# Kernel tuning notes

Measured on AMD Instinct MI355X. Metric: run time of the kernel, lower is better.

## Reference

```python
import jax, jax.numpy as jnp
import numpy as np

D = 256          # d_model
NPRE = 16; NMLP = 16; NPOST = 16
K = 4            # top_k
P = NPRE * NMLP * NPOST   # 4096 pathways
HMAX = 5 * D     # max mlp expert hidden width (padded storage)
B, S = 8, 256


def _gelu(z):
    return jax.nn.gelu(z, approximate=False)  # torch nn.GELU default = exact erf


def _ln(z, g, b, eps=1e-5):
    mu = z.mean(-1, keepdims=True)
    v = ((z - mu) ** 2).mean(-1, keepdims=True)
    return (z - mu) * jax.lax.rsqrt(v + eps) * g + b


def setup_inputs() -> dict:
    key = jax.random.key(0)
    ks = jax.random.split(key, 8)

    def nrm(k, shape, scale):
        return jax.random.normal(k, shape, dtype=jnp.float32) * scale

    return {
        "x": nrm(ks[0], (B, S, D), 1.0),
        # router MLP (dropout inactive in eval)
        "rw1": nrm(ks[1], (D, 256), D ** -0.5), "rb1": jnp.zeros((256,), jnp.float32),
        "rw2": nrm(ks[2], (256, 128), 256 ** -0.5), "rb2": jnp.zeros((128,), jnp.float32),
        "rw3": nrm(ks[3], (128, P), 128 ** -0.5), "rb3": jnp.zeros((P,), jnp.float32),
        "temp": jnp.ones((1,), jnp.float32),
        # pre experts: Linear + LayerNorm + act
        "pw": nrm(ks[4], (NPRE, D, D), D ** -0.5), "pb": jnp.zeros((NPRE, D), jnp.float32),
        "pg": jnp.ones((NPRE, D), jnp.float32), "pbb": jnp.zeros((NPRE, D), jnp.float32),
        # mlp experts: variable hidden D*(2+i//4), padded to HMAX (unused cols sliced off)
        "mw1": nrm(ks[5], (NMLP, D, HMAX), D ** -0.5), "mb1": jnp.zeros((NMLP, HMAX), jnp.float32),
        "mw2": nrm(ks[6], (NMLP, HMAX, D), HMAX ** -0.5), "mb2": jnp.zeros((NMLP, D), jnp.float32),
        # post experts: Linear + (LayerNorm if even)
        "qw": nrm(ks[7], (NPOST, D, D), D ** -0.5), "qb": jnp.zeros((NPOST, D), jnp.float32),
        "qg": jnp.ones((NPOST, D), jnp.float32), "qbb": jnp.zeros((NPOST, D), jnp.float32),
    }


def reference(x, rw1, rb1, rw2, rb2, rw3, rb3, temp, pw, pb, pg, pbb,
              mw1, mb1, mw2, mb2, qw, qb, qg, qbb):
    Bv, Sv, Dv = x.shape
    N = Bv * Sv
    xt = x.reshape(N, Dv)

    # ---- router ----
    h = _gelu(xt @ rw1 + rb1)
    h = _gelu(h @ rw2 + rb2)
    scores = h @ rw3 + rb3                                  # [N, P]

    # ---- GLBL load-balance loss (softmax without temperature; torch.var unbiased) ----
    freq = jax.nn.softmax(scores, axis=-1).mean(0)          # [P]
    glbl_loss = P * jnp.var(freq, ddof=1)

    # ---- top-k pathway selection ----
    probs = jax.nn.softmax(scores / temp[0], axis=-1)
    top_vals, top_idx = jax.lax.top_k(probs, K)             # [N, K]
    pw_full = jnp.zeros((N, P), x.dtype).at[jnp.arange(N)[:, None], top_idx].set(top_vals)
    pathway_weights = pw_full / (pw_full.sum(-1, keepdims=True) + 1e-8)

    # ---- decompose pathway index -> (pre, mlp, post) ----
    pre_idx = top_idx // (NMLP * NPOST)
    rem = top_idx % (NMLP * NPOST)
    mlp_idx = rem // NPOST
    post_idx = rem % NPOST

    # ---- pre experts: compute all, gather per (token, slot) ----
    acts = [_gelu, jax.nn.relu, jnp.tanh]
    pre_all = jnp.stack(
        [acts[i % 3](_ln(xt @ pw[i] + pb[i], pg[i], pbb[i])) for i in range(NPRE)],
        axis=1)                                              # [N, NPRE, D]
    x_pre = jnp.take_along_axis(pre_all, pre_idx[:, :, None], axis=1)  # [N, K, D]

    # ---- mlp experts (variable hidden width), masked combine ----
    x_mlp = jnp.zeros_like(x_pre)
    for j in range(NMLP):
        hid = Dv * (2 + j // 4)
        a = _gelu if j % 2 == 0 else jax.nn.relu
        mid = a(jnp.einsum('nkd,dh->nkh', x_pre, mw1[j, :, :hid]) + mb1[j, :hid])
        out = jnp.einsum('nkh,hd->nkd', mid, mw2[j, :hid, :]) + mb2[j]
        x_mlp = x_mlp + jnp.where((mlp_idx == j)[:, :, None], out, 0.0)

    # ---- post experts, masked combine ----
    x_post = jnp.zeros_like(x_mlp)
    for q in range(NPOST):
        out = jnp.einsum('nkd,de->nke', x_mlp, qw[q]) + qb[q]
        if q % 2 == 0:
            out = _ln(out, qg[q], qbb[q])
        x_post = x_post + jnp.where((post_idx == q)[:, :, None], out, 0.0)

    # original weights each pathway by its (unnormalized) top value
    output = (x_post * top_vals[:, :, None]).sum(1).reshape(Bv, Sv, Dv)
    return output, glbl_loss, pathway_weights.reshape(Bv, Sv, P)
```

## Files before the change

### kernel.cpp

```cpp
#include <hip/hip_runtime.h>
#include <math.h>

#define DMODEL 256
#define PWAYS  4096
#define TOPK   4
#define HMAX   1280
#define NTOK   2048
#define NPAIR  (NTOK*TOPK)
#define FSLOTS 16
#define TILE   16
#define YBLK   64
#define MROWS  64
#define YMLP   8
#define CTOT   56

typedef __attribute__((ext_vector_type(8))) short bf16x8;
typedef __attribute__((ext_vector_type(8))) unsigned short u16x8;
typedef __attribute__((ext_vector_type(4))) float f32x4;

#define MFMA_BF16 __builtin_amdgcn_mfma_f32_16x16x32_bf16

__device__ __forceinline__ float gelu_exact(float z) {
    return 0.5f * z * (1.0f + erff(z * 0.70710678118654752440f));
}

__device__ __forceinline__ unsigned short f32_to_bf16_rne(float f) {
    unsigned u = __float_as_uint(f);
    unsigned r = u + 0x7FFFu + ((u >> 16) & 1u);
    return (unsigned short)(r >> 16);
}

__device__ __forceinline__ float bf16_to_f32(unsigned short h) {
    return __uint_as_float((unsigned)h << 16);
}

__device__ __forceinline__ int chunk_base(int e) {
    int g = e >> 2, r = e & 3;
    return 4 * (2 * g + (g * (g - 1)) / 2) + r * (2 + g);
}


__global__ void k_zero(float* __restrict__ pwout, float* __restrict__ freq_part) {
    const int i = blockIdx.x * 256 + threadIdx.x;
    const int stride = gridDim.x * 256;
    for (int j = i; j < NTOK * PWAYS; j += stride) pwout[j] = 0.0f;
    for (int j = i; j < FSLOTS * PWAYS; j += stride) freq_part[j] = 0.0f;
}

__global__ void k_zero2(float* __restrict__ out, float* __restrict__ x_mlp,
                        int* __restrict__ cnts) {
    const int i = blockIdx.x * 256 + threadIdx.x;
    const int stride = gridDim.x * 256;
    for (int j = i; j < NTOK * DMODEL; j += stride) out[j] = 0.0f;
    for (int j = i; j < NPAIR * DMODEL; j += stride) x_mlp[j] = 0.0f;
    if (i < 192) cnts[i] = 0;
}

__global__ void __launch_bounds__(256) k_router_h(
    const float* __restrict__ x,
    const float* __restrict__ rw1, const float* __restrict__ rb1,
    const float* __restrict__ rw2, const float* __restrict__ rb2,
    unsigned short* __restrict__ h2h, unsigned short* __restrict__ h2l) {
    __shared__ float xs[4][DMODEL];
    __shared__ float h1s[4][DMODEL];
    __shared__ float h2s[4][128];
    const int tid = threadIdx.x;
    const int n0 = blockIdx.x * 4;

    for (int idx = tid; idx < 4 * DMODEL; idx += 256)
        xs[idx >> 8][idx & 255] = x[(size_t)n0 * DMODEL + idx];
    __syncthreads();

    {
        float bias = rb1[tid];
        float a0 = bias, a1 = bias, a2 = bias, a3 = bias;
        for (int c = 0; c < DMODEL; c++) {
            float wv = rw1[c * DMODEL + tid];
            a0 += xs[0][c] * wv; a1 += xs[1][c] * wv;
            a2 += xs[2][c] * wv; a3 += xs[3][c] * wv;
        }
        h1s[0][tid] = gelu_exact(a0); h1s[1][tid] = gelu_exact(a1);
        h1s[2][tid] = gelu_exact(a2); h1s[3][tid] = gelu_exact(a3);
    }
    __syncthreads();

    {
        const int col = tid & 127;
        const int pr = tid >> 7;
        float bias = rb2[col];
        float b0 = bias, b1 = bias;
        for (int c = 0; c < DMODEL; c++) {
            float wv = rw2[c * 128 + col];
            b0 += h1s[2 * pr + 0][c] * wv;
            b1 += h1s[2 * pr + 1][c] * wv;
        }
        h2s[2 * pr + 0][col] = gelu_exact(b0);
        h2s[2 * pr + 1][col] = gelu_exact(b1);
    }
    __syncthreads();

    for (int idx = tid; idx < 512; idx += 256) {
        const int t = idx >> 7, col = idx & 127;
        const float v = h2s[t][col];
        const unsigned short h = f32_to_bf16_rne(v);
        const size_t o = (size_t)(n0 + t) * 128 + col;
        h2h[o] = h;
        h2l[o] = f32_to_bf16_rne(v - bf16_to_f32(h));
    }
}

__global__ void __launch_bounds__(256) k_pack3(
    const float* __restrict__ rw3, unsigned short* __restrict__ P3) {
    const int nb = blockIdx.x;
    const int tid = threadIdx.x;
    const int kb = tid >> 6, lane = tid & 63;
    const int l15 = lane & 15, lhi = lane >> 4;
    const int k0 = kb * 32 + lhi * 8;
    const int n = nb * 16 + l15;
    u16x8 hv, lv;
#pragma unroll
    for (int j = 0; j < 8; ++j) {
        const float f = rw3[(size_t)(k0 + j) * PWAYS + n];
        const unsigned short h = f32_to_bf16_rne(f);
        hv[j] = h;
        lv[j] = f32_to_bf16_rne(f - bf16_to_f32(h));
    }
    const size_t o0 = ((size_t)(0 * 256 + nb) * 4 + kb) * 512 + (size_t)lane * 8;
    const size_t o1 = ((size_t)(1 * 256 + nb) * 4 + kb) * 512 + (size_t)lane * 8;
    *(u16x8*)&P3[o0] = hv;
    *(u16x8*)&P3[o1] = lv;
}

__global__ void __launch_bounds__(256, 2) k_scores(
    const unsigned short* __restrict__ h2h, const unsigned short* __restrict__ h2l,
    const unsigned short* __restrict__ P3, const float* __restrict__ rb3,
    float* __restrict__ scores) {
    const int n0 = blockIdx.x * 32;
    const int by = blockIdx.y;
    const int tid = threadIdx.x;
    const int wid = tid >> 6, lane = tid & 63;
    const int l15 = lane & 15, lhi = lane >> 4;

    __shared__ unsigned short ah[32][136];
    __shared__ unsigned short al[32][136];

    for (int t = tid; t < 512; t += 256) {
        const int row = t >> 4, seg = (t & 15) * 8;
        const size_t g = (size_t)(n0 + row) * 128 + seg;
        *(u16x8*)&ah[row][seg] = *(const u16x8*)&h2h[g];
        *(u16x8*)&al[row][seg] = *(const u16x8*)&h2l[g];
    }
    __syncthreads();

    f32x4 acc[2][4];
    const f32x4 zf = {0.f, 0.f, 0.f, 0.f};
#pragma unroll
    for (int ms = 0; ms < 2; ++ms)
#pragma unroll
        for (int ns = 0; ns < 4; ++ns) acc[ms][ns] = zf;

#pragma unroll 1
    for (int kb = 0; kb < 4; ++kb) {
        const int ko = kb * 32 + lhi * 8;
        const bf16x8 a_h0 = *(const bf16x8*)&ah[l15][ko];
        const bf16x8 a_h1 = *(const bf16x8*)&ah[16 + l15][ko];
        const bf16x8 a_l0 = *(const bf16x8*)&al[l15][ko];
        const bf16x8 a_l1 = *(const bf16x8*)&al[16 + l15][ko];
#pragma unroll
        for (int ns = 0; ns < 4; ++ns) {
            const int nb = by * 16 + wid * 4 + ns;
            const size_t bo = ((size_t)nb * 4 + kb) * 512 + (size_t)lane * 8;
            const bf16x8 bh = *(const bf16x8*)&P3[bo];
            const bf16x8 bl = *(const bf16x8*)&P3[bo + 524288];
            acc[0][ns] = MFMA_BF16(a_h0, bh, acc[0][ns], 0, 0, 0);
            acc[1][ns] = MFMA_BF16(a_h1, bh, acc[1][ns], 0, 0, 0);
            acc[0][ns] = MFMA_BF16(a_l0, bh, acc[0][ns], 0, 0, 0);
            acc[1][ns] = MFMA_BF16(a_l1, bh, acc[1][ns], 0, 0, 0);
            acc[0][ns] = MFMA_BF16(a_h0, bl, acc[0][ns], 0, 0, 0);
            acc[1][ns] = MFMA_BF16(a_h1, bl, acc[1][ns], 0, 0, 0);
        }
    }

#pragma unroll
    for (int ms = 0; ms < 2; ++ms)
#pragma unroll
        for (int ns = 0; ns < 4; ++ns) {
            const int col = by * 256 + wid * 64 + ns * 16 + l15;
            const float bias = rb3[col];
#pragma unroll
            for (int r = 0; r < 4; ++r) {
                const int row = n0 + ms * 16 + lhi * 4 + r;
                scores[(size_t)row * PWAYS + col] = acc[ms][ns][r] + bias;
            }
        }
}

__global__ void __launch_bounds__(256) k_topk(
    const float* __restrict__ scores, const float* __restrict__ temp,
    int* __restrict__ top_idx, float* __restrict__ top_vals,
    float* __restrict__ pw_out, float* __restrict__ tok_m, float* __restrict__ tok_i) {
    const int n = blockIdx.x;
    const int tid = threadIdx.x;
    const int wid = tid >> 6, lane = tid & 63;
    const float* row = scores + (size_t)n * PWAYS;

    float sv[16];
#pragma unroll
    for (int i = 0; i < 16; ++i) sv[i] = row[tid + i * 256];

    __shared__ float wred[4];
    __shared__ float wr1[4], wrT[4];
    __shared__ float wbv[4];
    __shared__ int wbi[4];
    __shared__ int sel[TOPK];
    __shared__ float selv[TOPK];

    float lmax = -3.402823466e38f;
#pragma unroll
    for (int i = 0; i < 16; ++i) lmax = fmaxf(lmax, sv[i]);
    for (int o = 32; o > 0; o >>= 1) lmax = fmaxf(lmax, __shfl_down(lmax, o));
    if (lane == 0) wred[wid] = lmax;
    __syncthreads();
    const float m = fmaxf(fmaxf(wred[0], wred[1]), fmaxf(wred[2], wred[3]));

    const float invT = 1.0f / temp[0];
    float e1 = 0.f, eT = 0.f;
#pragma unroll
    for (int i = 0; i < 16; ++i) {
        const float d = sv[i] - m;
        e1 += expf(d);
        eT += expf(d * invT);
    }
    for (int o = 32; o > 0; o >>= 1) { e1 += __shfl_down(e1, o); eT += __shfl_down(eT, o); }
    if (lane == 0) { wr1[wid] = e1; wrT[wid] = eT; }
    __syncthreads();
    const float sum1 = wr1[0] + wr1[1] + wr1[2] + wr1[3];
    const float sumT = wrT[0] + wrT[1] + wrT[2] + wrT[3];

    for (int r = 0; r < TOPK; ++r) {
        float bv = -3.402823466e38f;
        int bi = PWAYS;
#pragma unroll
        for (int i = 0; i < 16; ++i) {
            const int p = tid + i * 256;
            bool skip = false;
            for (int u = 0; u < r; ++u) if (sel[u] == p) skip = true;
            if (!skip && sv[i] > bv) { bv = sv[i]; bi = p; }
        }
        for (int o = 32; o > 0; o >>= 1) {
            const float ov = __shfl_down(bv, o);
            const int oi = __shfl_down(bi, o);
            if (ov > bv || (ov == bv && oi < bi)) { bv = ov; bi = oi; }
        }
        if (lane == 0) { wbv[wid] = bv; wbi[wid] = bi; }
        __syncthreads();
        if (tid == 0) {
            float b = wbv[0]; int bidx = wbi[0];
            for (int w = 1; w < 4; ++w)
                if (wbv[w] > b || (wbv[w] == b && wbi[w] < bidx)) { b = wbv[w]; bidx = wbi[w]; }
            sel[r] = bidx; selv[r] = b;
        }
        __syncthreads();
    }

    if (tid == 0) {
        float tv[TOPK];
        float wsum = 1e-8f;
#pragma unroll
        for (int k2 = 0; k2 < TOPK; ++k2) {
            tv[k2] = expf((selv[k2] - m) * invT) / sumT;
            wsum += tv[k2];
        }
        const float invw = 1.0f / wsum;
#pragma unroll
        for (int k2 = 0; k2 < TOPK; ++k2) {
            top_idx[n * TOPK + k2] = sel[k2];
            top_vals[n * TOPK + k2] = tv[k2];
            pw_out[(size_t)n * PWAYS + sel[k2]] = tv[k2] * invw;
        }
        tok_m[n] = m;
        tok_i[n] = 1.0f / sum1;
    }
}

__global__ void __launch_bounds__(256) k_freq(
    const float* __restrict__ scores, const float* __restrict__ tok_m,
    const float* __restrict__ tok_i, float* __restrict__ freq_part) {
    const int bx = blockIdx.x;
    const int by = blockIdx.y;
    const int tid = threadIdx.x;
    const int wid = tid >> 6, lane = tid & 63;
    const int col = bx * 64 + lane;

    float acc = 0.f;
    const int r0 = by * 128;
    for (int r = r0 + wid; r < r0 + 128; r += 4) {
        const float mm = tok_m[r], iv = tok_i[r];
        acc += expf(scores[(size_t)r * PWAYS + col] - mm) * iv;
    }
    __shared__ float fs[4][64];
    fs[wid][lane] = acc;
    __syncthreads();
    if (wid == 0)
        freq_part[(size_t)by * PWAYS + col] = fs[0][lane] + fs[1][lane] + fs[2][lane] + fs[3][lane];
}

__global__ void k_freq_loss(const float* __restrict__ freq_part, float* __restrict__ out_loss) {
    __shared__ float fl[PWAYS];
    __shared__ float red[256];
    const int tid = threadIdx.x;
    for (int p = tid; p < PWAYS; p += 256) {
        float s = 0.f;
        for (int sl = 0; sl < FSLOTS; sl++) s += freq_part[(size_t)sl * PWAYS + p];
        fl[p] = s * (1.0f / NTOK);
    }
    __syncthreads();
    float s = 0.f;
    for (int p = tid; p < PWAYS; p += 256) s += fl[p];
    red[tid] = s; __syncthreads();
    for (int st = 128; st > 0; st >>= 1) { if (tid < st) red[tid] += red[tid + st]; __syncthreads(); }
    const float mu = red[0] * (1.0f / PWAYS);
    __syncthreads();
    float ss = 0.f;
    for (int p = tid; p < PWAYS; p += 256) {
        float d = fl[p] - mu;
        ss += d * d;
    }
    red[tid] = ss; __syncthreads();
    for (int st = 128; st > 0; st >>= 1) { if (tid < st) red[tid] += red[tid + st]; __syncthreads(); }
    if (tid == 0)
        out_loss[0] = (float)PWAYS * red[0] / (float)(PWAYS - 1);
}


__global__ void k_count(const int* __restrict__ top_idx, int* __restrict__ counts) {
    const int p = blockIdx.x * 256 + threadIdx.x;
    if (p >= NPAIR) return;
    const int idx = top_idx[p];
    atomicAdd(&counts[0 * 16 + (idx >> 8)], 1);
    atomicAdd(&counts[1 * 16 + ((idx >> 4) & 15)], 1);
    atomicAdd(&counts[2 * 16 + (idx & 15)], 1);
}

__global__ void k_prefix(const int* __restrict__ counts, int* __restrict__ offsets,
                         int* __restrict__ cursors) {
    if (threadIdx.x != 0 || blockIdx.x != 0) return;
    for (int s = 0; s < 3; s++) {
        int run = 0;
        for (int e = 0; e < 16; e++) {
            offsets[s * 16 + e] = run;
            cursors[s * 16 + e] = run;
            run += counts[s * 16 + e];
        }
    }
}

__global__ void k_scatter(const int* __restrict__ top_idx, int* __restrict__ cursors,
                          int* __restrict__ lists) {
    const int p = blockIdx.x * 256 + threadIdx.x;
    if (p >= NPAIR) return;
    const int idx = top_idx[p];
    int pos;
    pos = atomicAdd(&cursors[0 * 16 + (idx >> 8)], 1);        lists[0 * NPAIR + pos] = p;
    pos = atomicAdd(&cursors[1 * 16 + ((idx >> 4) & 15)], 1); lists[1 * NPAIR + pos] = p;
    pos = atomicAdd(&cursors[2 * 16 + (idx & 15)], 1);        lists[2 * NPAIR + pos] = p;
}

__device__ __forceinline__ void wave_stats(const float* row, int lane,
                                           float& s1, float& s2) {
    float v0 = row[lane], v1 = row[lane + 64], v2 = row[lane + 128], v3 = row[lane + 192];
    s1 = v0 + v1 + v2 + v3;
    s2 = v0 * v0 + v1 * v1 + v2 * v2 + v3 * v3;
    for (int o = 32; o > 0; o >>= 1) {
        s1 += __shfl_down(s1, o);
        s2 += __shfl_down(s2, o);
    }
}

__global__ void __launch_bounds__(256) k_packw(
    const float* __restrict__ mw1, const float* __restrict__ mw2,
    unsigned short* __restrict__ W1P, unsigned short* __restrict__ W2P) {
    const int cl = blockIdx.x;
    const int which = blockIdx.y;
    const int kb = blockIdx.z;
    int e = 0;
    while (e < 15 && chunk_base(e + 1) <= cl) ++e;
    const int ch = cl - chunk_base(e);
    const int hbase = ch * 256;
    const int tid = threadIdx.x;
    const int wid = tid >> 6, lane = tid & 63;
    const int l15 = lane & 15, lhi = lane >> 4;

    unsigned short* dst = which ? W2P : W1P;

    for (int nb = wid; nb < 16; nb += 4) {
        const int n = nb * 16 + l15;
        const int k0 = kb * 32 + lhi * 8;
        u16x8 hv, lv;
#pragma unroll
        for (int j = 0; j < 8; ++j) {
            float f;
            if (which == 0)
                f = mw1[((size_t)e * DMODEL + (k0 + j)) * HMAX + hbase + n];
            else
                f = mw2[((size_t)e * HMAX + hbase + k0 + j) * DMODEL + n];
            const unsigned short h = f32_to_bf16_rne(f);
            hv[j] = h;
            lv[j] = f32_to_bf16_rne(f - bf16_to_f32(h));
        }
        const size_t o0 = ((((size_t)cl * 2 + 0) * 16 + nb) * 8 + kb) * 512 + (size_t)lane * 8;
        const size_t o1 = ((((size_t)cl * 2 + 1) * 16 + nb) * 8 + kb) * 512 + (size_t)lane * 8;
        *(u16x8*)&dst[o0] = hv;
        *(u16x8*)&dst[o1] = lv;
    }
}

__global__ void __launch_bounds__(256, 8) k_pre(
    const float* __restrict__ x, const float* __restrict__ pw, const float* __restrict__ pb,
    const float* __restrict__ pg, const float* __restrict__ pbb,
    const int* __restrict__ counts, const int* __restrict__ offsets,
    const int* __restrict__ lists,
    unsigned short* __restrict__ x_h, unsigned short* __restrict__ x_l) {
    const int e = blockIdx.x;
    const int cnt = counts[e];
    const int off = offsets[e];
    const int tid = threadIdx.x;
    const float bias = pb[e * DMODEL + tid];
    const float g = pg[e * DMODEL + tid], bb = pbb[e * DMODEL + tid];
    const int am = e % 3;
    const float* W = pw + (size_t)e * DMODEL * DMODEL + tid;

    __shared__ int prs[TILE];
    __shared__ float buf[TILE][DMODEL];
    __shared__ float mus[TILE], ivs[TILE];

    for (int base = blockIdx.y * TILE; base < cnt; base += YBLK * TILE) {
        const int Tact = min(TILE, cnt - base);
        if (tid < TILE) prs[tid] = lists[off + base + ((tid < Tact) ? tid : (Tact - 1))];
        __syncthreads();
#pragma unroll
        for (int j = 0; j < TILE; j++)
            buf[j][tid] = x[(size_t)(prs[j] >> 2) * DMODEL + tid];
        __syncthreads();

        float acc[TILE];
#pragma unroll
        for (int j = 0; j < TILE; j++) acc[j] = bias;
        for (int c = 0; c < DMODEL; c += 4) {
            const float w0 = W[(c + 0) * DMODEL], w1 = W[(c + 1) * DMODEL];
            const float w2 = W[(c + 2) * DMODEL], w3 = W[(c + 3) * DMODEL];
#pragma unroll
            for (int j = 0; j < TILE; j++) {
                float4 xv = *(const float4*)&buf[j][c];
                acc[j] += xv.x * w0 + xv.y * w1 + xv.z * w2 + xv.w * w3;
            }
        }
        __syncthreads();
#pragma unroll
        for (int j = 0; j < TILE; j++) buf[j][tid] = acc[j];
        __syncthreads();

        const int w = tid >> 6, lane = tid & 63;
        for (int i = 0; i < 4; i++) {
            const int j = w * 4 + i;
            float s1, s2;
            wave_stats(buf[j], lane, s1, s2);
            if (lane == 0) {
                float mu = s1 * (1.0f / DMODEL);
                mus[j] = mu;
                ivs[j] = rsqrtf(s2 * (1.0f / DMODEL) - mu * mu + 1e-5f);
            }
        }
        __syncthreads();

        for (int j = 0; j < Tact; j++) {
            float y = (acc[j] - mus[j]) * ivs[j] * g + bb;
            y = (am == 0) ? gelu_exact(y) : (am == 1 ? fmaxf(y, 0.f) : tanhf(y));
            const unsigned short h = f32_to_bf16_rne(y);
            const size_t o = (size_t)prs[j] * DMODEL + tid;
            x_h[o] = h;
            x_l[o] = f32_to_bf16_rne(y - bf16_to_f32(h));
        }
        __syncthreads();
    }
}

__global__ void __launch_bounds__(256, 2) k_mlp_mfma(
    const unsigned short* __restrict__ x_h, const unsigned short* __restrict__ x_l,
    const unsigned short* __restrict__ W1P, const unsigned short* __restrict__ W2P,
    const float* __restrict__ mb1, const float* __restrict__ mb2,
    const int* __restrict__ counts, const int* __restrict__ offsets,
    const int* __restrict__ lists, float* __restrict__ x_mlp) {
    const int p = blockIdx.x & 7;
    const int j = blockIdx.x >> 3;
    const int ea = p;
    const int eb = (p < 4) ? (p + 12) : (p + 4);
    const int na = (2 + (ea >> 2)) * YMLP;
    int e, ch, y;
    if (j < na) { e = ea; ch = j >> 3; y = j & 7; }
    else        { e = eb; ch = (j - na) >> 3; y = (j - na) & 7; }

    const int cnt = counts[16 + e];
    if (cnt == 0) return;
    const int off = offsets[16 + e];
    const int cl = chunk_base(e) + ch;
    const bool is_gelu = ((e & 1) == 0);
    const int tid = threadIdx.x;
    const int wid = tid >> 6, lane = tid & 63;
    const int l15 = lane & 15, lhi = lane >> 4;

    __shared__ int prs[MROWS];
    __shared__ unsigned short ah[MROWS][264];
    __shared__ unsigned short al[MROWS][264];

    float hb_s[4], ob_s[4];
#pragma unroll
    for (int ns = 0; ns < 4; ++ns) {
        const int col = wid * 64 + ns * 16 + l15;
        hb_s[ns] = mb1[e * HMAX + ch * DMODEL + col];
        ob_s[ns] = (ch == 0) ? mb2[e * DMODEL + col] : 0.0f;
    }

    const size_t wbase = (size_t)cl * 2 * 65536;

    for (int base = y * MROWS; base < cnt; base += YMLP * MROWS) {
        const int Tact = min(MROWS, cnt - base);
        if (tid < MROWS) prs[tid] = lists[NPAIR + off + base + min(tid, Tact - 1)];
        __syncthreads();
        for (int t = tid; t < 2048; t += 256) {
            const int row = t >> 5, seg = (t & 31) * 8;
            const size_t gsrc = (size_t)prs[row] * DMODEL + seg;
            *(uint4*)&ah[row][seg] = *(const uint4*)&x_h[gsrc];
            *(uint4*)&al[row][seg] = *(const uint4*)&x_l[gsrc];
        }
        __syncthreads();

        {
            f32x4 acc[4][4];
            const f32x4 zf = {0.f, 0.f, 0.f, 0.f};
#pragma unroll
            for (int ms = 0; ms < 4; ++ms)
#pragma unroll
                for (int ns = 0; ns < 4; ++ns) acc[ms][ns] = zf;

#pragma unroll 1
            for (int kb = 0; kb < 8; ++kb) {
                const int ko = kb * 32 + lhi * 8;
#pragma unroll
                for (int ns = 0; ns < 4; ++ns) {
                    const size_t bo = wbase + (size_t)(((wid * 4 + ns) * 8 + kb) * 512 + lane * 8);
                    const bf16x8 bh = *(const bf16x8*)&W1P[bo];
                    const bf16x8 bl = *(const bf16x8*)&W1P[bo + 65536];
#pragma unroll
                    for (int ms = 0; ms < 4; ++ms) {
                        const bf16x8 a_h = *(const bf16x8*)&ah[ms * 16 + l15][ko];
                        const bf16x8 a_l = *(const bf16x8*)&al[ms * 16 + l15][ko];
                        acc[ms][ns] = MFMA_BF16(a_h, bh, acc[ms][ns], 0, 0, 0);
                        acc[ms][ns] = MFMA_BF16(a_l, bh, acc[ms][ns], 0, 0, 0);
                        acc[ms][ns] = MFMA_BF16(a_h, bl, acc[ms][ns], 0, 0, 0);
                    }
                }
            }
            __syncthreads();

#pragma unroll
            for (int ms = 0; ms < 4; ++ms)
#pragma unroll
                for (int ns = 0; ns < 4; ++ns) {
                    const int col = wid * 64 + ns * 16 + l15;
#pragma unroll
                    for (int r = 0; r < 4; ++r) {
                        const int row = ms * 16 + lhi * 4 + r;
                        float v = acc[ms][ns][r] + hb_s[ns];
                        v = is_gelu ? gelu_exact(v) : fmaxf(v, 0.0f);
                        const unsigned short h = f32_to_bf16_rne(v);
                        ah[row][col] = h;
                        al[row][col] = f32_to_bf16_rne(v - bf16_to_f32(h));
                    }
                }
            __syncthreads();
        }

        {
            f32x4 acc2[4][4];
            const f32x4 zf = {0.f, 0.f, 0.f, 0.f};
#pragma unroll
            for (int ms = 0; ms < 4; ++ms)
#pragma unroll
                for (int ns = 0; ns < 4; ++ns) acc2[ms][ns] = zf;

#pragma unroll 1
            for (int kb = 0; kb < 8; ++kb) {
                const int ko = kb * 32 + lhi * 8;
#pragma unroll
                for (int ns = 0; ns < 4; ++ns) {
                    const size_t bo = wbase + (size_t)(((wid * 4 + ns) * 8 + kb) * 512 + lane * 8);
                    const bf16x8 bh = *(const bf16x8*)&W2P[bo];
                    const bf16x8 bl = *(const bf16x8*)&W2P[bo + 65536];
#pragma unroll
                    for (int ms = 0; ms < 4; ++ms) {
                        const bf16x8 a_h = *(const bf16x8*)&ah[ms * 16 + l15][ko];
                        const bf16x8 a_l = *(const bf16x8*)&al[ms * 16 + l15][ko];
                        acc2[ms][ns] = MFMA_BF16(a_h, bh, acc2[ms][ns], 0, 0, 0);
                        acc2[ms][ns] = MFMA_BF16(a_l, bh, acc2[ms][ns], 0, 0, 0);
                        acc2[ms][ns] = MFMA_BF16(a_h, bl, acc2[ms][ns], 0, 0, 0);
                    }
                }
            }

#pragma unroll
            for (int ms = 0; ms < 4; ++ms)
#pragma unroll
                for (int ns = 0; ns < 4; ++ns) {
                    const int col = wid * 64 + ns * 16 + l15;
#pragma unroll
                    for (int r = 0; r < 4; ++r) {
                        const int row = ms * 16 + lhi * 4 + r;
                        if (row < Tact)
                            atomicAdd(&x_mlp[(size_t)prs[row] * DMODEL + col],
                                      acc2[ms][ns][r] + ob_s[ns]);
                    }
                }
        }
        __syncthreads();
    }
}

__global__ void __launch_bounds__(256, 8) k_post(
    const float* __restrict__ x_mlp,
    const float* __restrict__ qw, const float* __restrict__ qb,
    const float* __restrict__ qg, const float* __restrict__ qbb,
    const float* __restrict__ top_val,
    const int* __restrict__ counts, const int* __restrict__ offsets,
    const int* __restrict__ lists, float* __restrict__ out) {
    const int e = blockIdx.x;
    const int cnt = counts[32 + e];
    const int off = offsets[32 + e];
    const int tid = threadIdx.x;
    const float bias = qb[e * DMODEL + tid];
    const bool has_ln = ((e & 1) == 0);
    const float g = has_ln ? qg[e * DMODEL + tid] : 0.f;
    const float bb = has_ln ? qbb[e * DMODEL + tid] : 0.f;
    const float* W = qw + (size_t)e * DMODEL * DMODEL + tid;

    __shared__ int prs[TILE];
    __shared__ float tvs[TILE];
    __shared__ float buf[TILE][DMODEL];
    __shared__ float mus[TILE], ivs[TILE];

    for (int base = blockIdx.y * TILE; base < cnt; base += YBLK * TILE) {
        const int Tact = min(TILE, cnt - base);
        if (tid < TILE) {
            int p = lists[2 * NPAIR + off + base + ((tid < Tact) ? tid : (Tact - 1))];
            prs[tid] = p;
            tvs[tid] = top_val[p];
        }
        __syncthreads();
#pragma unroll
        for (int j = 0; j < TILE; j++)
            buf[j][tid] = x_mlp[(size_t)prs[j] * DMODEL + tid];
        __syncthreads();

        float acc[TILE];
#pragma unroll
        for (int j = 0; j < TILE; j++) acc[j] = bias;
        for (int c = 0; c < DMODEL; c += 4) {
            const float w0 = W[(c + 0) * DMODEL], w1 = W[(c + 1) * DMODEL];
            const float w2 = W[(c + 2) * DMODEL], w3 = W[(c + 3) * DMODEL];
#pragma unroll
            for (int j = 0; j < TILE; j++) {
                float4 xv = *(const float4*)&buf[j][c];
                acc[j] += xv.x * w0 + xv.y * w1 + xv.z * w2 + xv.w * w3;
            }
        }

        if (has_ln) {
            __syncthreads();
#pragma unroll
            for (int j = 0; j < TILE; j++) buf[j][tid] = acc[j];
            __syncthreads();
            const int w = tid >> 6, lane = tid & 63;
            for (int i = 0; i < 4; i++) {
                const int j = w * 4 + i;
                float s1, s2;
                wave_stats(buf[j], lane, s1, s2);
                if (lane == 0) {
                    float mu = s1 * (1.0f / DMODEL);
                    mus[j] = mu;
                    ivs[j] = rsqrtf(s2 * (1.0f / DMODEL) - mu * mu + 1e-5f);
                }
            }
            __syncthreads();
            for (int j = 0; j < Tact; j++) {
                float t = (acc[j] - mus[j]) * ivs[j] * g + bb;
                atomicAdd(&out[(size_t)(prs[j] >> 2) * DMODEL + tid], tvs[j] * t);
            }
        } else {
            for (int j = 0; j < Tact; j++)
                atomicAdd(&out[(size_t)(prs[j] >> 2) * DMODEL + tid], tvs[j] * acc[j]);
        }
        __syncthreads();
    }
}

extern "C" void kernel_launch(void* const* d_in, const int* in_sizes, int n_in,
                              void* d_out, int out_size, void* d_ws, size_t ws_size,
                              hipStream_t stream) {
    (void)in_sizes; (void)n_in; (void)out_size; (void)ws_size;

    const float* x    = (const float*)d_in[0];
    const float* rw1  = (const float*)d_in[1];
    const float* rb1  = (const float*)d_in[2];
    const float* rw2  = (const float*)d_in[3];
    const float* rb2  = (const float*)d_in[4];
    const float* rw3  = (const float*)d_in[5];
    const float* rb3  = (const float*)d_in[6];
    const float* temp = (const float*)d_in[7];
    const float* pw   = (const float*)d_in[8];
    const float* pb   = (const float*)d_in[9];
    const float* pg   = (const float*)d_in[10];
    const float* pbb  = (const float*)d_in[11];
    const float* mw1  = (const float*)d_in[12];
    const float* mb1  = (const float*)d_in[13];
    const float* mw2  = (const float*)d_in[14];
    const float* mb2  = (const float*)d_in[15];
    const float* qw   = (const float*)d_in[16];
    const float* qb   = (const float*)d_in[17];
    const float* qg   = (const float*)d_in[18];
    const float* qbb  = (const float*)d_in[19];

    float* out      = (float*)d_out;
    float* out_loss = out + (size_t)NTOK * DMODEL;
    float* out_pw   = out_loss + 1;

    float* freq_part = (float*)d_ws;
    int*   top_idx   = (int*)(freq_part + (size_t)FSLOTS * PWAYS);
    float* top_val   = (float*)(top_idx + NPAIR);
    int*   counts    = (int*)(top_val + NPAIR);
    int*   offsets   = counts + 64;
    int*   cursors   = offsets + 64;
    int*   lists     = cursors + 64;
    float* x_mlp     = (float*)(lists + 3 * NPAIR);
    unsigned short* x_h = (unsigned short*)(x_mlp + (size_t)NPAIR * DMODEL);
    unsigned short* x_l = x_h + (size_t)NPAIR * DMODEL;
    unsigned short* W1P = x_l + (size_t)NPAIR * DMODEL;
    unsigned short* W2P = W1P + (size_t)CTOT * 2 * 65536;
    unsigned short* P3  = W2P + (size_t)CTOT * 2 * 65536;
    unsigned short* h2h = P3 + 2 * 524288;
    unsigned short* h2l = h2h + (size_t)NTOK * 128;
    float* tok_m = (float*)(h2l + (size_t)NTOK * 128);
    float* tok_i = tok_m + NTOK;
    float* scores = x_mlp;

    k_zero<<<1024, 256, 0, stream>>>(out_pw, freq_part);
    k_router_h<<<NTOK / 4, 256, 0, stream>>>(x, rw1, rb1, rw2, rb2, h2h, h2l);
    k_pack3<<<256, 256, 0, stream>>>(rw3, P3);
    k_scores<<<dim3(64, 16), 256, 0, stream>>>(h2h, h2l, P3, rb3, scores);
    k_topk<<<NTOK, 256, 0, stream>>>(scores, temp, top_idx, top_val, out_pw, tok_m, tok_i);
    k_freq<<<dim3(64, 16), 256, 0, stream>>>(scores, tok_m, tok_i, freq_part);
    k_freq_loss<<<1, 256, 0, stream>>>(freq_part, out_loss);

    k_zero2<<<1024, 256, 0, stream>>>(out, x_mlp, counts);
    k_count<<<NPAIR / 256, 256, 0, stream>>>(top_idx, counts);
    k_prefix<<<1, 64, 0, stream>>>(counts, offsets, cursors);
    k_scatter<<<NPAIR / 256, 256, 0, stream>>>(top_idx, cursors, lists);
    k_packw<<<dim3(CTOT, 2, 8), 256, 0, stream>>>(mw1, mw2, W1P, W2P);
    k_pre<<<dim3(16, YBLK), 256, 0, stream>>>(x, pw, pb, pg, pbb,
                                              counts, offsets, lists, x_h, x_l);
    k_mlp_mfma<<<CTOT * YMLP, 256, 0, stream>>>(x_h, x_l, W1P, W2P, mb1, mb2,
                                                counts, offsets, lists, x_mlp);
    k_post<<<dim3(16, YBLK), 256, 0, stream>>>(x_mlp, qw, qb, qg, qbb, top_val,
                                               counts, offsets, lists, out);
}
```

Baseline: 542.9 us.

## Move pre and post expert GEMMs onto bf16 split-precision MFMA

```diff
diff --git a/kernel.cpp b/kernel.cpp
--- a/kernel.cpp
+++ b/kernel.cpp
@@ -8,8 +8,6 @@
 #define NTOK   2048
 #define NPAIR  (NTOK*TOPK)
 #define FSLOTS 16
-#define TILE   16
-#define YBLK   64
 #define MROWS  64
 #define YMLP   8
 #define CTOT   56
@@ -60,15 +58,21 @@
     const float* __restrict__ x,
     const float* __restrict__ rw1, const float* __restrict__ rb1,
     const float* __restrict__ rw2, const float* __restrict__ rb2,
-    unsigned short* __restrict__ h2h, unsigned short* __restrict__ h2l) {
+    unsigned short* __restrict__ h2h, unsigned short* __restrict__ h2l,
+    unsigned short* __restrict__ xth, unsigned short* __restrict__ xtl) {
     __shared__ float xs[4][DMODEL];
     __shared__ float h1s[4][DMODEL];
     __shared__ float h2s[4][128];
     const int tid = threadIdx.x;
     const int n0 = blockIdx.x * 4;
 
-    for (int idx = tid; idx < 4 * DMODEL; idx += 256)
-        xs[idx >> 8][idx & 255] = x[(size_t)n0 * DMODEL + idx];
+    for (int idx = tid; idx < 4 * DMODEL; idx += 256) {
+        const float v = x[(size_t)n0 * DMODEL + idx];
+        xs[idx >> 8][idx & 255] = v;
+        const unsigned short h = f32_to_bf16_rne(v);
+        xth[(size_t)n0 * DMODEL + idx] = h;
+        xtl[(size_t)n0 * DMODEL + idx] = f32_to_bf16_rne(v - bf16_to_f32(h));
+    }
     __syncthreads();
 
     {
@@ -129,6 +133,36 @@
     const size_t o1 = ((size_t)(1 * 256 + nb) * 4 + kb) * 512 + (size_t)lane * 8;
     *(u16x8*)&P3[o0] = hv;
     *(u16x8*)&P3[o1] = lv;
+}
+
+__global__ void __launch_bounds__(256) k_packq(
+    const float* __restrict__ pw, const float* __restrict__ qw,
+    unsigned short* __restrict__ PPK, unsigned short* __restrict__ QPK) {
+    const int e = blockIdx.x;
+    const int which = blockIdx.y;
+    const int kb = blockIdx.z;
+    const int tid = threadIdx.x;
+    const int wid = tid >> 6, lane = tid & 63;
+    const int l15 = lane & 15, lhi = lane >> 4;
+    const float* src = which ? qw : pw;
+    unsigned short* dst = which ? QPK : PPK;
+
+    for (int nb = wid; nb < 16; nb += 4) {
+        const int n = nb * 16 + l15;
+        const int k0 = kb * 32 + lhi * 8;
+        u16x8 hv, lv;
+#pragma unroll
+        for (int j = 0; j < 8; ++j) {
+            const float f = src[(size_t)e * DMODEL * DMODEL + (size_t)(k0 + j) * DMODEL + n];
+            const unsigned short h = f32_to_bf16_rne(f);
+            hv[j] = h;
+            lv[j] = f32_to_bf16_rne(f - bf16_to_f32(h));
+        }
+        const size_t o0 = ((((size_t)e * 2 + 0) * 16 + nb) * 8 + kb) * 512 + (size_t)lane * 8;
+        const size_t o1 = ((((size_t)e * 2 + 1) * 16 + nb) * 8 + kb) * 512 + (size_t)lane * 8;
+        *(u16x8*)&dst[o0] = hv;
+        *(u16x8*)&dst[o1] = lv;
+    }
 }
 
 __global__ void __launch_bounds__(256, 2) k_scores(
@@ -366,17 +400,6 @@
     pos = atomicAdd(&cursors[2 * 16 + (idx & 15)], 1);        lists[2 * NPAIR + pos] = p;
 }
 
-__device__ __forceinline__ void wave_stats(const float* row, int lane,
-                                           float& s1, float& s2) {
-    float v0 = row[lane], v1 = row[lane + 64], v2 = row[lane + 128], v3 = row[lane + 192];
-    s1 = v0 + v1 + v2 + v3;
-    s2 = v0 * v0 + v1 * v1 + v2 * v2 + v3 * v3;
-    for (int o = 32; o > 0; o >>= 1) {
-        s1 += __shfl_down(s1, o);
-        s2 += __shfl_down(s2, o);
-    }
-}
-
 __global__ void __launch_bounds__(256) k_packw(
     const float* __restrict__ mw1, const float* __restrict__ mw2,
     unsigned short* __restrict__ W1P, unsigned short* __restrict__ W2P) {
@@ -415,72 +438,141 @@
     }
 }
 
-__global__ void __launch_bounds__(256, 8) k_pre(
-    const float* __restrict__ x, const float* __restrict__ pw, const float* __restrict__ pb,
-    const float* __restrict__ pg, const float* __restrict__ pbb,
+__global__ void __launch_bounds__(256) k_cvt(
+    const float* __restrict__ src, unsigned short* __restrict__ dh,
+    unsigned short* __restrict__ dl) {
+    const size_t i = ((size_t)blockIdx.x * 256 + threadIdx.x) * 4;
+    const float4 v = *(const float4*)&src[i];
+    ushort4 hv, lv;
+    hv.x = f32_to_bf16_rne(v.x); lv.x = f32_to_bf16_rne(v.x - bf16_to_f32(hv.x));
+    hv.y = f32_to_bf16_rne(v.y); lv.y = f32_to_bf16_rne(v.y - bf16_to_f32(hv.y));
+    hv.z = f32_to_bf16_rne(v.z); lv.z = f32_to_bf16_rne(v.z - bf16_to_f32(hv.z));
+    hv.w = f32_to_bf16_rne(v.w); lv.w = f32_to_bf16_rne(v.w - bf16_to_f32(hv.w));
+    *(ushort4*)&dh[i] = hv;
+    *(ushort4*)&dl[i] = lv;
+}
+
+__global__ void __launch_bounds__(256, 2) k_pre_mfma(
+    const unsigned short* __restrict__ xth, const unsigned short* __restrict__ xtl,
+    const unsigned short* __restrict__ PPK,
+    const float* __restrict__ pb, const float* __restrict__ pg, const float* __restrict__ pbb,
     const int* __restrict__ counts, const int* __restrict__ offsets,
     const int* __restrict__ lists,
     unsigned short* __restrict__ x_h, unsigned short* __restrict__ x_l) {
     const int e = blockIdx.x;
     const int cnt = counts[e];
+    if (cnt == 0) return;
     const int off = offsets[e];
-    const int tid = threadIdx.x;
-    const float bias = pb[e * DMODEL + tid];
-    const float g = pg[e * DMODEL + tid], bb = pbb[e * DMODEL + tid];
     const int am = e % 3;
-    const float* W = pw + (size_t)e * DMODEL * DMODEL + tid;
-
-    __shared__ int prs[TILE];
-    __shared__ float buf[TILE][DMODEL];
-    __shared__ float mus[TILE], ivs[TILE];
-
-    for (int base = blockIdx.y * TILE; base < cnt; base += YBLK * TILE) {
-        const int Tact = min(TILE, cnt - base);
-        if (tid < TILE) prs[tid] = lists[off + base + ((tid < Tact) ? tid : (Tact - 1))];
-        __syncthreads();
-#pragma unroll
-        for (int j = 0; j < TILE; j++)
-            buf[j][tid] = x[(size_t)(prs[j] >> 2) * DMODEL + tid];
-        __syncthreads();
-
-        float acc[TILE];
-#pragma unroll
-        for (int j = 0; j < TILE; j++) acc[j] = bias;
-        for (int c = 0; c < DMODEL; c += 4) {
-            const float w0 = W[(c + 0) * DMODEL], w1 = W[(c + 1) * DMODEL];
-            const float w2 = W[(c + 2) * DMODEL], w3 = W[(c + 3) * DMODEL];
-#pragma unroll
-            for (int j = 0; j < TILE; j++) {
-                float4 xv = *(const float4*)&buf[j][c];
-                acc[j] += xv.x * w0 + xv.y * w1 + xv.z * w2 + xv.w * w3;
+    const int tid = threadIdx.x;
+    const int wid = tid >> 6, lane = tid & 63;
+    const int l15 = lane & 15, lhi = lane >> 4;
+
+    __shared__ int prs[32];
+    __shared__ unsigned short ah[32][264];
+    __shared__ unsigned short al[32][264];
+    __shared__ float s1s[4][32], s2s[4][32];
+    __shared__ float mus[32], ivs[32];
+
+    float bias4[4], g4[4], bb4[4];
+#pragma unroll
+    for (int ns = 0; ns < 4; ++ns) {
+        const int col = wid * 64 + ns * 16 + l15;
+        bias4[ns] = pb[e * DMODEL + col];
+        g4[ns] = pg[e * DMODEL + col];
+        bb4[ns] = pbb[e * DMODEL + col];
+    }
+    const size_t wbase = (size_t)e * 2 * 65536;
+
+    for (int base = blockIdx.y * 32; base < cnt; base += 16 * 32) {
+        const int Tact = min(32, cnt - base);
+        if (tid < 32) prs[tid] = lists[off + base + min(tid, Tact - 1)];
+        __syncthreads();
+        for (int t = tid; t < 1024; t += 256) {
+            const int row = t >> 5, seg = (t & 31) * 8;
+            const size_t gsrc = (size_t)(prs[row] >> 2) * DMODEL + seg;
+            *(uint4*)&ah[row][seg] = *(const uint4*)&xth[gsrc];
+            *(uint4*)&al[row][seg] = *(const uint4*)&xtl[gsrc];
+        }
+        __syncthreads();
+
+        f32x4 acc[2][4];
+        const f32x4 zf = {0.f, 0.f, 0.f, 0.f};
+#pragma unroll
+        for (int ms = 0; ms < 2; ++ms)
+#pragma unroll
+            for (int ns = 0; ns < 4; ++ns) acc[ms][ns] = zf;
+
+#pragma unroll 1
+        for (int kb = 0; kb < 8; ++kb) {
+            const int ko = kb * 32 + lhi * 8;
+            const bf16x8 a_h0 = *(const bf16x8*)&ah[l15][ko];
+            const bf16x8 a_h1 = *(const bf16x8*)&ah[16 + l15][ko];
+            const bf16x8 a_l0 = *(const bf16x8*)&al[l15][ko];
+            const bf16x8 a_l1 = *(const bf16x8*)&al[16 + l15][ko];
+#pragma unroll
+            for (int ns = 0; ns < 4; ++ns) {
+                const size_t bo = wbase + (size_t)(((wid * 4 + ns) * 8 + kb) * 512 + lane * 8);
+                const bf16x8 bh = *(const bf16x8*)&PPK[bo];
+                const bf16x8 bl = *(const bf16x8*)&PPK[bo + 65536];
+                acc[0][ns] = MFMA_BF16(a_h0, bh, acc[0][ns], 0, 0, 0);
+                acc[1][ns] = MFMA_BF16(a_h1, bh, acc[1][ns], 0, 0, 0);
+                acc[0][ns] = MFMA_BF16(a_l0, bh, acc[0][ns], 0, 0, 0);
+                acc[1][ns] = MFMA_BF16(a_l1, bh, acc[1][ns], 0, 0, 0);
+                acc[0][ns] = MFMA_BF16(a_h0, bl, acc[0][ns], 0, 0, 0);
+                acc[1][ns] = MFMA_BF16(a_h1, bl, acc[1][ns], 0, 0, 0);
             }
         }
-        __syncthreads();
-#pragma unroll
-        for (int j = 0; j < TILE; j++) buf[j][tid] = acc[j];
-        __syncthreads();
-
-        const int w = tid >> 6, lane = tid & 63;
-        for (int i = 0; i < 4; i++) {
-            const int j = w * 4 + i;
-            float s1, s2;
-            wave_stats(buf[j], lane, s1, s2);
-            if (lane == 0) {
-                float mu = s1 * (1.0f / DMODEL);
-                mus[j] = mu;
-                ivs[j] = rsqrtf(s2 * (1.0f / DMODEL) - mu * mu + 1e-5f);
+
+#pragma unroll
+        for (int ms = 0; ms < 2; ++ms)
+#pragma unroll
+            for (int r = 0; r < 4; ++r) {
+                float s1 = 0.f, s2 = 0.f;
+#pragma unroll
+                for (int ns = 0; ns < 4; ++ns) {
+                    const float v = acc[ms][ns][r] + bias4[ns];
+                    s1 += v; s2 += v * v;
+                }
+#pragma unroll
+                for (int o = 1; o < 16; o <<= 1) {
+                    s1 += __shfl_xor(s1, o);
+                    s2 += __shfl_xor(s2, o);
+                }
+                if (l15 == 0) {
+                    s1s[wid][ms * 16 + lhi * 4 + r] = s1;
+                    s2s[wid][ms * 16 + lhi * 4 + r] = s2;
+                }
             }
-        }
-        __syncthreads();
-
-        for (int j = 0; j < Tact; j++) {
-            float y = (acc[j] - mus[j]) * ivs[j] * g + bb;
-            y = (am == 0) ? gelu_exact(y) : (am == 1 ? fmaxf(y, 0.f) : tanhf(y));
-            const unsigned short h = f32_to_bf16_rne(y);
-            const size_t o = (size_t)prs[j] * DMODEL + tid;
-            x_h[o] = h;
-            x_l[o] = f32_to_bf16_rne(y - bf16_to_f32(h));
-        }
+        __syncthreads();
+        if (tid < 32) {
+            const float s1 = s1s[0][tid] + s1s[1][tid] + s1s[2][tid] + s1s[3][tid];
+            const float s2 = s2s[0][tid] + s2s[1][tid] + s2s[2][tid] + s2s[3][tid];
+            const float mu = s1 * (1.0f / DMODEL);
+            mus[tid] = mu;
+            ivs[tid] = rsqrtf(s2 * (1.0f / DMODEL) - mu * mu + 1e-5f);
+        }
+        __syncthreads();
+
+#pragma unroll
+        for (int ms = 0; ms < 2; ++ms)
+#pragma unroll
+            for (int ns = 0; ns < 4; ++ns) {
+                const int col = wid * 64 + ns * 16 + l15;
+#pragma unroll
+                for (int r = 0; r < 4; ++r) {
+                    const int row = ms * 16 + lhi * 4 + r;
+                    if (row < Tact) {
+                        const float v = acc[ms][ns][r] + bias4[ns];
+                        float y = (v - mus[row]) * ivs[row] * g4[ns] + bb4[ns];
+                        y = (am == 0) ? gelu_exact(y) : (am == 1 ? fmaxf(y, 0.f) : tanhf(y));
+                        const unsigned short h = f32_to_bf16_rne(y);
+                        const size_t o = (size_t)prs[row] * DMODEL + col;
+                        x_h[o] = h;
+                        x_l[o] = f32_to_bf16_rne(y - bf16_to_f32(h));
+                    }
+                }
+            }
         __syncthreads();
     }
 }
@@ -626,79 +718,130 @@
     }
 }
 
-__global__ void __launch_bounds__(256, 8) k_post(
-    const float* __restrict__ x_mlp,
-    const float* __restrict__ qw, const float* __restrict__ qb,
-    const float* __restrict__ qg, const float* __restrict__ qbb,
+__global__ void __launch_bounds__(256, 2) k_post_mfma(
+    const unsigned short* __restrict__ xmh, const unsigned short* __restrict__ xml,
+    const unsigned short* __restrict__ QPK,
+    const float* __restrict__ qb, const float* __restrict__ qg, const float* __restrict__ qbb,
     const float* __restrict__ top_val,
     const int* __restrict__ counts, const int* __restrict__ offsets,
     const int* __restrict__ lists, float* __restrict__ out) {
     const int e = blockIdx.x;
     const int cnt = counts[32 + e];
+    if (cnt == 0) return;
     const int off = offsets[32 + e];
-    const int tid = threadIdx.x;
-    const float bias = qb[e * DMODEL + tid];
     const bool has_ln = ((e & 1) == 0);
-    const float g = has_ln ? qg[e * DMODEL + tid] : 0.f;
-    const float bb = has_ln ? qbb[e * DMODEL + tid] : 0.f;
-    const float* W = qw + (size_t)e * DMODEL * DMODEL + tid;
-
-    __shared__ int prs[TILE];
-    __shared__ float tvs[TILE];
-    __shared__ float buf[TILE][DMODEL];
-    __shared__ float mus[TILE], ivs[TILE];
-
-    for (int base = blockIdx.y * TILE; base < cnt; base += YBLK * TILE) {
-        const int Tact = min(TILE, cnt - base);
-        if (tid < TILE) {
-            int p = lists[2 * NPAIR + off + base + ((tid < Tact) ? tid : (Tact - 1))];
+    const int tid = threadIdx.x;
+    const int wid = tid >> 6, lane = tid & 63;
+    const int l15 = lane & 15, lhi = lane >> 4;
+
+    __shared__ int prs[32];
+    __shared__ float tvs[32];
+    __shared__ unsigned short ah[32][264];
+    __shared__ unsigned short al[32][264];
+    __shared__ float s1s[4][32], s2s[4][32];
+    __shared__ float mus[32], ivs[32];
+
+    float bias4[4], g4[4], bb4[4];
+#pragma unroll
+    for (int ns = 0; ns < 4; ++ns) {
+        const int col = wid * 64 + ns * 16 + l15;
+        bias4[ns] = qb[e * DMODEL + col];
+        g4[ns] = qg[e * DMODEL + col];
+        bb4[ns] = qbb[e * DMODEL + col];
+    }
+    const size_t wbase = (size_t)e * 2 * 65536;
+
+    for (int base = blockIdx.y * 32; base < cnt; base += 16 * 32) {
+        const int Tact = min(32, cnt - base);
+        if (tid < 32) {
+            const int p = lists[2 * NPAIR + off + base + min(tid, Tact - 1)];
             prs[tid] = p;
             tvs[tid] = top_val[p];
         }
         __syncthreads();
-#pragma unroll
-        for (int j = 0; j < TILE; j++)
-            buf[j][tid] = x_mlp[(size_t)prs[j] * DMODEL + tid];
-        __syncthreads();
-
-        float acc[TILE];
-#pragma unroll
-        for (int j = 0; j < TILE; j++) acc[j] = bias;
-        for (int c = 0; c < DMODEL; c += 4) {
-            const float w0 = W[(c + 0) * DMODEL], w1 = W[(c + 1) * DMODEL];
-            const float w2 = W[(c + 2) * DMODEL], w3 = W[(c + 3) * DMODEL];
-#pragma unroll
-            for (int j = 0; j < TILE; j++) {
-                float4 xv = *(const float4*)&buf[j][c];
-                acc[j] += xv.x * w0 + xv.y * w1 + xv.z * w2 + xv.w * w3;
+        for (int t = tid; t < 1024; t += 256) {
+            const int row = t >> 5, seg = (t & 31) * 8;
+            const size_t gsrc = (size_t)prs[row] * DMODEL + seg;
+            *(uint4*)&ah[row][seg] = *(const uint4*)&xmh[gsrc];
+            *(uint4*)&al[row][seg] = *(const uint4*)&xml[gsrc];
+        }
+        __syncthreads();
+
+        f32x4 acc[2][4];
+        const f32x4 zf = {0.f, 0.f, 0.f, 0.f};
+#pragma unroll
+        for (int ms = 0; ms < 2; ++ms)
+#pragma unroll
+            for (int ns = 0; ns < 4; ++ns) acc[ms][ns] = zf;
+
+#pragma unroll 1
+        for (int kb = 0; kb < 8; ++kb) {
+            const int ko = kb * 32 + lhi * 8;
+            const bf16x8 a_h0 = *(const bf16x8*)&ah[l15][ko];
+            const bf16x8 a_h1 = *(const bf16x8*)&ah[16 + l15][ko];
+            const bf16x8 a_l0 = *(const bf16x8*)&al[l15][ko];
+            const bf16x8 a_l1 = *(const bf16x8*)&al[16 + l15][ko];
+#pragma unroll
+            for (int ns = 0; ns < 4; ++ns) {
+                const size_t bo = wbase + (size_t)(((wid * 4 + ns) * 8 + kb) * 512 + lane * 8);
+                const bf16x8 bh = *(const bf16x8*)&QPK[bo];
+                const bf16x8 bl = *(const bf16x8*)&QPK[bo + 65536];
+                acc[0][ns] = MFMA_BF16(a_h0, bh, acc[0][ns], 0, 0, 0);
+                acc[1][ns] = MFMA_BF16(a_h1, bh, acc[1][ns], 0, 0, 0);
+                acc[0][ns] = MFMA_BF16(a_l0, bh, acc[0][ns], 0, 0, 0);
+                acc[1][ns] = MFMA_BF16(a_l1, bh, acc[1][ns], 0, 0, 0);
+                acc[0][ns] = MFMA_BF16(a_h0, bl, acc[0][ns], 0, 0, 0);
+                acc[1][ns] = MFMA_BF16(a_h1, bl, acc[1][ns], 0, 0, 0);
             }
         }
 
         if (has_ln) {
+#pragma unroll
+            for (int ms = 0; ms < 2; ++ms)
+#pragma unroll
+                for (int r = 0; r < 4; ++r) {
+                    float s1 = 0.f, s2 = 0.f;
+#pragma unroll
+                    for (int ns = 0; ns < 4; ++ns) {
+                        const float v = acc[ms][ns][r] + bias4[ns];
+                        s1 += v; s2 += v * v;
+                    }
+#pragma unroll
+                    for (int o = 1; o < 16; o <<= 1) {
+                        s1 += __shfl_xor(s1, o);
+                        s2 += __shfl_xor(s2, o);
+                    }
+                    if (l15 == 0) {
+                        s1s[wid][ms * 16 + lhi * 4 + r] = s1;
+                        s2s[wid][ms * 16 + lhi * 4 + r] = s2;
+                    }
+                }
             __syncthreads();
-#pragma unroll
-            for (int j = 0; j < TILE; j++) buf[j][tid] = acc[j];
+            if (tid < 32) {
+                const float s1 = s1s[0][tid] + s1s[1][tid] + s1s[2][tid] + s1s[3][tid];
+                const float s2 = s2s[0][tid] + s2s[1][tid] + s2s[2][tid] + s2s[3][tid];
+                const float mu = s1 * (1.0f / DMODEL);
+                mus[tid] = mu;
+                ivs[tid] = rsqrtf(s2 * (1.0f / DMODEL) - mu * mu + 1e-5f);
+            }
             __syncthreads();
-            const int w = tid >> 6, lane = tid & 63;
-            for (int i = 0; i < 4; i++) {
-                const int j = w * 4 + i;
-                float s1, s2;
-                wave_stats(buf[j], lane, s1, s2);
-                if (lane == 0) {
-                    float mu = s1 * (1.0f / DMODEL);
-                    mus[j] = mu;
-                    ivs[j] = rsqrtf(s2 * (1.0f / DMODEL) - mu * mu + 1e-5f);
+        }
+
+#pragma unroll
+        for (int ms = 0; ms < 2; ++ms)
+#pragma unroll
+            for (int ns = 0; ns < 4; ++ns) {
+                const int col = wid * 64 + ns * 16 + l15;
+#pragma unroll
+                for (int r = 0; r < 4; ++r) {
+                    const int row = ms * 16 + lhi * 4 + r;
+                    if (row < Tact) {
+                        const float v = acc[ms][ns][r] + bias4[ns];
+                        const float t = has_ln ? ((v - mus[row]) * ivs[row] * g4[ns] + bb4[ns]) : v;
+                        atomicAdd(&out[(size_t)(prs[row] >> 2) * DMODEL + col], tvs[row] * t);
+                    }
                 }
             }
-            __syncthreads();
-            for (int j = 0; j < Tact; j++) {
-                float t = (acc[j] - mus[j]) * ivs[j] * g + bb;
-                atomicAdd(&out[(size_t)(prs[j] >> 2) * DMODEL + tid], tvs[j] * t);
-            }
-        } else {
-            for (int j = 0; j < Tact; j++)
-                atomicAdd(&out[(size_t)(prs[j] >> 2) * DMODEL + tid], tvs[j] * acc[j]);
-        }
         __syncthreads();
     }
 }
@@ -750,11 +893,18 @@
     unsigned short* h2l = h2h + (size_t)NTOK * 128;
     float* tok_m = (float*)(h2l + (size_t)NTOK * 128);
     float* tok_i = tok_m + NTOK;
+    unsigned short* xth = (unsigned short*)(tok_i + NTOK);
+    unsigned short* xtl = xth + (size_t)NTOK * DMODEL;
+    unsigned short* xmh = xtl + (size_t)NTOK * DMODEL;
+    unsigned short* xml = xmh + (size_t)NPAIR * DMODEL;
+    unsigned short* PPK = xml + (size_t)NPAIR * DMODEL;
+    unsigned short* QPK = PPK + (size_t)16 * 2 * 65536;
     float* scores = x_mlp;
 
     k_zero<<<1024, 256, 0, stream>>>(out_pw, freq_part);
-    k_router_h<<<NTOK / 4, 256, 0, stream>>>(x, rw1, rb1, rw2, rb2, h2h, h2l);
+    k_router_h<<<NTOK / 4, 256, 0, stream>>>(x, rw1, rb1, rw2, rb2, h2h, h2l, xth, xtl);
     k_pack3<<<256, 256, 0, stream>>>(rw3, P3);
+    k_packq<<<dim3(16, 2, 8), 256, 0, stream>>>(pw, qw, PPK, QPK);
     k_scores<<<dim3(64, 16), 256, 0, stream>>>(h2h, h2l, P3, rb3, scores);
     k_topk<<<NTOK, 256, 0, stream>>>(scores, temp, top_idx, top_val, out_pw, tok_m, tok_i);
     k_freq<<<dim3(64, 16), 256, 0, stream>>>(scores, tok_m, tok_i, freq_part);
@@ -765,10 +915,11 @@
     k_prefix<<<1, 64, 0, stream>>>(counts, offsets, cursors);
     k_scatter<<<NPAIR / 256, 256, 0, stream>>>(top_idx, cursors, lists);
     k_packw<<<dim3(CTOT, 2, 8), 256, 0, stream>>>(mw1, mw2, W1P, W2P);
-    k_pre<<<dim3(16, YBLK), 256, 0, stream>>>(x, pw, pb, pg, pbb,
-                                              counts, offsets, lists, x_h, x_l);
+    k_pre_mfma<<<dim3(16, 16), 256, 0, stream>>>(xth, xtl, PPK, pb, pg, pbb,
+                                                 counts, offsets, lists, x_h, x_l);
     k_mlp_mfma<<<CTOT * YMLP, 256, 0, stream>>>(x_h, x_l, W1P, W2P, mb1, mb2,
                                                 counts, offsets, lists, x_mlp);
-    k_post<<<dim3(16, YBLK), 256, 0, stream>>>(x_mlp, qw, qb, qg, qbb, top_val,
-                                               counts, offsets, lists, out);
-}
+    k_cvt<<<NPAIR * DMODEL / 1024, 256, 0, stream>>>(x_mlp, xmh, xml);
+    k_post_mfma<<<dim3(16, 16), 256, 0, stream>>>(xmh, xml, QPK, qb, qg, qbb, top_val,
+                                                  counts, offsets, lists, out);
+}
```

Measured after the change: 518.8 us. -4.4%, faster.
